# Kernel optimization log

Hardware: AMD Instinct MI355X
Metric: run time of the kernel (lower is better)

## Reference

```python
import jax, jax.numpy as jnp
import numpy as np

NEG_SLOPE = 0.2  # GAT LeakyReLU slope
EPS = 1e-16


def _pagat_conv(x, path_index, W, a, b, heads, out_ch, concat):
    """Path-augmented GAT conv: attention over (head, mid, tail) path triples,
    messages flow tail -> head, softmax-normalized per destination node."""
    N = x.shape[0]
    head, mid, tail = path_index[0], path_index[1], path_index[2]
    h = (x @ W).reshape(N, heads, out_ch)            # [N, H, C]
    # attention logits from all three path positions: [P, H]
    e = (jnp.einsum('phc,hc->ph', h[head], a[0])
         + jnp.einsum('phc,hc->ph', h[mid], a[1])
         + jnp.einsum('phc,hc->ph', h[tail], a[2]))
    e = jax.nn.leaky_relu(e, NEG_SLOPE)
    # segment softmax over paths grouped by destination (head) node
    m = jax.ops.segment_max(e, head, num_segments=N)  # [N, H]
    ex = jnp.exp(e - m[head])
    s = jax.ops.segment_sum(ex, head, num_segments=N)  # [N, H]
    alpha = ex / (s[head] + EPS)                       # [P, H]
    # aggregate tail features weighted by attention
    out = jax.ops.segment_sum(alpha[..., None] * h[tail], head, num_segments=N)  # [N, H, C]
    if concat:
        out = out.reshape(N, heads * out_ch)
    else:
        out = out.mean(axis=1)
    return out + b


def setup_inputs() -> dict:
    key = jax.random.key(0)
    ks = jax.random.split(key, 8)
    N, F_in, H, C, CLS, P = 100000, 500, 8, 16, 16, 1000000
    x = jax.random.normal(ks[0], (N, F_in), dtype=jnp.float32)
    path_index = jax.random.randint(ks[1], (3, P), 0, N, dtype=jnp.int32)
    W1 = jax.random.normal(ks[2], (F_in, H * C), dtype=jnp.float32) * 0.05
    a1 = jax.random.normal(ks[3], (3, H, C), dtype=jnp.float32) * 0.05
    b1 = jnp.zeros((H * C,), dtype=jnp.float32)
    W2 = jax.random.normal(ks[4], (H * C, CLS), dtype=jnp.float32) * 0.05
    a2 = jax.random.normal(ks[5], (3, 1, CLS), dtype=jnp.float32) * 0.05
    b2 = jnp.zeros((CLS,), dtype=jnp.float32)
    return {"x": x, "path_index": path_index, "W1": W1, "a1": a1, "b1": b1,
            "W2": W2, "a2": a2, "b2": b2}


def reference(x, path_index, W1, a1, b1, W2, a2, b2):
    # eval mode: dropout is identity
    h = _pagat_conv(x, path_index, W1, a1, b1, heads=8, out_ch=16, concat=True)
    h = jax.nn.elu(h)
    h = _pagat_conv(h, path_index, W2, a2, b2, heads=1, out_ch=16, concat=False)
    return jax.nn.log_softmax(h, axis=1)
```

## Files before the change

### kernel.cpp

```cpp
#include <hip/hip_runtime.h>
#include <hip/hip_bf16.h>

#define F_IN  500
#define HC    128
#define NHEAD 8
#define CDIM  16
#define NCLS  16
#define KPAD  512

static __device__ __forceinline__ float bf(const __hip_bfloat16 v) {
    return __bfloat162float(v);
}

static __device__ __forceinline__ unsigned int enc_f32(float f) {
    unsigned int u = __float_as_uint(f);
    return (u & 0x80000000u) ? ~u : (u | 0x80000000u);
}
static __device__ __forceinline__ float dec_f32(unsigned int u) {
    return __uint_as_float((u & 0x80000000u) ? (u & 0x7FFFFFFFu) : ~u);
}

typedef __bf16 bf16x8 __attribute__((ext_vector_type(8)));
typedef float f32x4 __attribute__((ext_vector_type(4)));

static __device__ __forceinline__ void gload16(const void* g, void* l) {
    __builtin_amdgcn_global_load_lds(
        (const __attribute__((address_space(1))) void*)g,
        (__attribute__((address_space(3))) void*)l, 16, 0, 0);
}

static __device__ __forceinline__ unsigned ldsoff(const void* p) {
    return (unsigned)(size_t)(const __attribute__((address_space(3))) void*)p;
}

static __device__ __forceinline__ void ds_read_f4(unsigned addr, float4& out) {
    asm volatile("ds_read_b128 %0, %1" : "=v"(out) : "v"(addr) : "memory");
}

template<int OFF>
static __device__ __forceinline__ bf16x8 gld_b(const __bf16* p) {
    bf16x8 o;
    asm volatile("global_load_dwordx4 %0, %1, off offset:%2"
                 : "=v"(o) : "v"(p), "i"(OFF) : "memory");
    return o;
}

__global__ void prep_kernel(const float* __restrict__ W1,
                            __bf16* __restrict__ w1t_hi,
                            __bf16* __restrict__ w1t_lo,
                            int* __restrict__ zp, int nz)
{
    int e = blockIdx.x * 256 + threadIdx.x;
    if (e < HC * KPAD) {
        int j = e & 7, lane = (e >> 3) & 63, ct = (e >> 9) & 3;
        int t = (e >> 11) & 15, wc = (e >> 15) & 1;
        int c = wc * 64 + ct * 16 + (lane & 15);
        int k = t * 32 + (lane >> 4) * 8 + j;
        float v = (k < F_IN) ? W1[k * HC + c] : 0.f;
        __bf16 h = (__bf16)v;
        w1t_hi[e] = h;
        w1t_lo[e] = (__bf16)(v - (float)h);
    }
    if (e < nz) zp[e] = 0;
}

static __device__ __forceinline__ void split8(const float4 a, const float4 b,
                                              bf16x8& hi, bf16x8& lo) {
    float v[8] = {a.x, a.y, a.z, a.w, b.x, b.y, b.z, b.w};
#pragma unroll
    for (int j = 0; j < 8; j++) {
        __bf16 h = (__bf16)v[j];
        hi[j] = h;
        lo[j] = (__bf16)(v[j] - (float)h);
    }
}

__global__ __launch_bounds__(256, 3) void gemm1_v7(
    const float* __restrict__ x,
    const __bf16* __restrict__ w1hi, const __bf16* __restrict__ w1lo,
    const float* __restrict__ zpad,
    __hip_bfloat16* __restrict__ h1,
    const int* __restrict__ pidx, int* __restrict__ deg, int N, int P)
{
    __shared__ float As[4][64 * 32];

    const int tid = threadIdx.x;
    const int lane = tid & 63, wave = tid >> 6;
    const int m = lane & 15, q = lane >> 4;
    const int wr = wave >> 1, wc = wave & 1;
    const int n0 = blockIdx.x * 64;
    const int woff = wave << 10;

    auto stage = [&](int buf, int t) {
        const int k0 = t * 32;
#pragma unroll
        for (int j = 0; j < 2; ++j) {
            int idx = j * 256 + tid;
            int r = idx >> 3, ps = idx & 7;
            int ls = ps ^ (r & 7);
            int kk = k0 + ls * 4;
            int grow = n0 + r;
            const float* src = (kk < F_IN)
                ? (x + (size_t)(grow < N ? grow : 0) * F_IN + kk)
                : zpad;
            gload16(src, (char*)&As[buf][0] + j * 4096 + woff);
        }
    };

    const __bf16* bh_base = w1hi + (size_t)wc * 32768 + (size_t)lane * 8;
    const __bf16* bl_base = w1lo + (size_t)wc * 32768 + (size_t)lane * 8;

    auto loadB = [&](bf16x8 (&bh)[4], bf16x8 (&bl)[4], int t) {
        const __bf16* ph = bh_base + (size_t)t * 2048;
        const __bf16* pl = bl_base + (size_t)t * 2048;
        bh[0] = gld_b<0>(ph);    bh[1] = gld_b<1024>(ph);
        bh[2] = gld_b<2048>(ph); bh[3] = gld_b<3072>(ph);
        bl[0] = gld_b<0>(pl);    bl[1] = gld_b<1024>(pl);
        bl[2] = gld_b<2048>(pl); bl[3] = gld_b<3072>(pl);
    };

    unsigned abase[4];
#pragma unroll
    for (int i = 0; i < 4; ++i) abase[i] = ldsoff(&As[i][0]);
    unsigned aoffs[2][2];
#pragma unroll
    for (int rt = 0; rt < 2; ++rt) {
        int r = wr * 32 + rt * 16 + m, x7 = r & 7;
        aoffs[rt][0] = r * 128 + (((2 * q) ^ x7) << 4);
        aoffs[rt][1] = r * 128 + (((2 * q + 1) ^ x7) << 4);
    }

    f32x4 acc[2][4];
#pragma unroll
    for (int rt = 0; rt < 2; ++rt)
#pragma unroll
        for (int ct = 0; ct < 4; ++ct) acc[rt][ct] = (f32x4){0.f, 0.f, 0.f, 0.f};

    bf16x8 bhA[4], blA[4], bhB[4], blB[4];

    stage(0, 0);
    stage(1, 1);
    loadB(bhA, blA, 0);
    stage(2, 2);

    auto compute = [&](bf16x8 (&bh)[4], bf16x8 (&bl)[4],
                       bf16x8 (&ah)[2], bf16x8 (&al)[2]) {
        __builtin_amdgcn_s_setprio(1);
#pragma unroll
        for (int rt = 0; rt < 2; ++rt)
#pragma unroll
            for (int ct = 0; ct < 4; ++ct) {
                acc[rt][ct] = __builtin_amdgcn_mfma_f32_16x16x32_bf16(ah[rt], bh[ct], acc[rt][ct], 0, 0, 0);
                acc[rt][ct] = __builtin_amdgcn_mfma_f32_16x16x32_bf16(ah[rt], bl[ct], acc[rt][ct], 0, 0, 0);
                acc[rt][ct] = __builtin_amdgcn_mfma_f32_16x16x32_bf16(al[rt], bh[ct], acc[rt][ct], 0, 0, 0);
            }
        __builtin_amdgcn_s_setprio(0);
    };

#pragma unroll
    for (int t = 0; t < 16; ++t) {
        if (t > 0) __builtin_amdgcn_s_barrier();
        if (t + 1 < 16) {
            if ((t & 1) == 0) loadB(bhB, blB, t + 1);
            else              loadB(bhA, blA, t + 1);
        }
        if (t + 3 < 16) stage((t + 3) & 3, t + 3);

        if (t <= 12)      asm volatile("s_waitcnt vmcnt(12)" ::: "memory");
        else if (t == 13) asm volatile("s_waitcnt vmcnt(10)" ::: "memory");
        else if (t == 14) asm volatile("s_waitcnt vmcnt(8)" ::: "memory");
        else              asm volatile("s_waitcnt vmcnt(0)" ::: "memory");
        __builtin_amdgcn_s_barrier();

        const int cur = t & 3;
        float4 fa[2][2];
        ds_read_f4(abase[cur] + aoffs[0][0], fa[0][0]);
        ds_read_f4(abase[cur] + aoffs[0][1], fa[0][1]);
        ds_read_f4(abase[cur] + aoffs[1][0], fa[1][0]);
        ds_read_f4(abase[cur] + aoffs[1][1], fa[1][1]);
        asm volatile("s_waitcnt lgkmcnt(0)" ::: "memory");
        __builtin_amdgcn_sched_barrier(0);

        bf16x8 ah[2], al[2];
        split8(fa[0][0], fa[0][1], ah[0], al[0]);
        split8(fa[1][0], fa[1][1], ah[1], al[1]);

        if ((t & 1) == 0) compute(bhA, blA, ah, al);
        else              compute(bhB, blB, ah, al);
    }

#pragma unroll
    for (int rt = 0; rt < 2; ++rt) {
        int rbase = n0 + wr * 32 + rt * 16 + q * 4;
#pragma unroll
        for (int ct = 0; ct < 4; ++ct) {
            int col = wc * 64 + ct * 16 + m;
#pragma unroll
            for (int r = 0; r < 4; ++r) {
                int row = rbase + r;
                if (row < N)
                    h1[(size_t)row * HC + col] = __float2bfloat16(acc[rt][ct][r]);
            }
        }
    }

    const int gsz = gridDim.x * 256;
    for (int i = blockIdx.x * 256 + tid; i < P; i += gsz)
        atomicAdd(deg + pidx[i], 1);
}

__global__ void dots1_kernel(const __hip_bfloat16* __restrict__ h1,
                             const float* __restrict__ a1,
                             float* __restrict__ d1,
                             unsigned int* __restrict__ gmax, int N)
{
    __shared__ unsigned int sm[16];
    if (threadIdx.x < 16) sm[threadIdx.x] = 0;
    __syncthreads();
    int id = blockIdx.x * blockDim.x + threadIdx.x;
    if (id < N * NHEAD) {
        int n = id >> 3, h = id & 7;
        const __hip_bfloat16* hp = h1 + (size_t)n * HC + h * CDIM;
        bf16x8 v0 = *(const bf16x8*)hp;
        bf16x8 v1 = *(const bf16x8*)(hp + 8);
        float s0 = 0.f, s1 = 0.f, s2 = 0.f;
#pragma unroll
        for (int c = 0; c < CDIM; c++) {
            float v = (c < 8) ? (float)v0[c & 7] : (float)v1[c & 7];
            s0 += v * a1[(0 * NHEAD + h) * CDIM + c];
            s1 += v * a1[(1 * NHEAD + h) * CDIM + c];
            s2 += v * a1[(2 * NHEAD + h) * CDIM + c];
        }
        d1[id] = s0;
        d1[N * NHEAD + id] = s1;
        d1[2 * N * NHEAD + id] = s2;
        atomicMax(&sm[h], enc_f32(s1));
        atomicMax(&sm[8 + h], enc_f32(s2));
    }
    __syncthreads();
    if (threadIdx.x < 16) atomicMax(&gmax[threadIdx.x], sm[threadIdx.x]);
}

__global__ void scan1_kernel(const int* __restrict__ deg, int* __restrict__ start,
                             int* __restrict__ bsum, int N) {
    __shared__ int sh[256];
    int i = blockIdx.x * 256 + threadIdx.x;
    int v = (i < N) ? deg[i] : 0;
    sh[threadIdx.x] = v;
    __syncthreads();
#pragma unroll
    for (int off = 1; off < 256; off <<= 1) {
        int x = (threadIdx.x >= off) ? sh[threadIdx.x - off] : 0;
        __syncthreads();
        sh[threadIdx.x] += x;
        __syncthreads();
    }
    if (i < N) start[i] = sh[threadIdx.x] - v;
    if (threadIdx.x == 255) bsum[blockIdx.x] = sh[255];
}

__global__ void scan2_kernel(int* __restrict__ bsum, int nb) {
    __shared__ int sh[512];
    int v = (threadIdx.x < nb) ? bsum[threadIdx.x] : 0;
    sh[threadIdx.x] = v;
    __syncthreads();
#pragma unroll
    for (int off = 1; off < 512; off <<= 1) {
        int x = (threadIdx.x >= off) ? sh[threadIdx.x - off] : 0;
        __syncthreads();
        sh[threadIdx.x] += x;
        __syncthreads();
    }
    if (threadIdx.x < nb) bsum[threadIdx.x] = sh[threadIdx.x] - v;
}

__global__ void scan3_kernel(int* __restrict__ start, const int* __restrict__ bsum, int N) {
    int i = blockIdx.x * 256 + threadIdx.x;
    if (i < N) start[i] += bsum[blockIdx.x];
}

__global__ void scatter_kernel(const int* __restrict__ pidx,
                               const int* __restrict__ start,
                               int* __restrict__ cursor,
                               int* __restrict__ csr, int P) {
    int p = blockIdx.x * blockDim.x + threadIdx.x;
    if (p >= P) return;
    int hd = pidx[p];
    int pos = atomicAdd(cursor + hd, 1);
    csr[start[hd] + pos] = p;
}

__global__ __launch_bounds__(256) void attn1_csr_kernel(
    const int* __restrict__ csr, const int* __restrict__ start,
    const int* __restrict__ deg, const int* __restrict__ pidx,
    const float* __restrict__ d1, const __hip_bfloat16* __restrict__ h1,
    const float* __restrict__ b1, const unsigned int* __restrict__ gmax,
    float* __restrict__ elu_out, int N, int P)
{
    int node = blockIdx.x * 4 + (threadIdx.x >> 6);
    if (node >= N) return;
    int lane = threadIdx.x & 63;
    int h = lane >> 3;
    int s0 = start[node], dg = deg[node];
    const float* d1m = d1 + (size_t)N * NHEAD;
    const float* d1t = d1 + (size_t)2 * N * NHEAD;
    const float dh = d1[node * NHEAD + h];
    float zub = dh + dec_f32(gmax[h]) + dec_f32(gmax[8 + h]);
    const float mxub = zub > 0.f ? zub : 0.2f * zub;

    float acc0 = 0.f, acc1 = 0.f, den = 0.f;
    for (int k0 = 0; k0 < dg; k0 += 8) {
        int kk = k0 + (lane & 7);
        bool valid = kk < dg;
        int p = csr[s0 + (valid ? kk : dg - 1)];
        int mid = pidx[P + p], tl = pidx[2 * P + p];
        float z = dh + d1m[mid * NHEAD + h] + d1t[tl * NHEAD + h];
        float e = z > 0.f ? z : 0.2f * z;
        float ex = valid ? __expf(e - mxub) : 0.f;
        den += ex;
        __hip_bfloat162 v[8];
        float exs[8];
#pragma unroll
        for (int dk = 0; dk < 8; dk++) {
            int tl_b = __shfl(tl, dk, 8);
            exs[dk] = __shfl(ex, dk, 8);
            v[dk] = *(const __hip_bfloat162*)(h1 + (size_t)tl_b * HC + 2 * lane);
        }
#pragma unroll
        for (int dk = 0; dk < 8; dk++) {
            acc0 += exs[dk] * bf(v[dk].x);
            acc1 += exs[dk] * bf(v[dk].y);
        }
    }
#pragma unroll
    for (int w = 1; w < 8; w <<= 1) den += __shfl_xor(den, w, 8);

    float inv = 1.f / (den + 1e-16f);
    int j0 = 2 * lane;
    float v0 = acc0 * inv + b1[j0];
    float v1 = acc1 * inv + b1[j0 + 1];
    v0 = v0 > 0.f ? v0 : __expf(v0) - 1.f;
    v1 = v1 > 0.f ? v1 : __expf(v1) - 1.f;
    *(float2*)(elu_out + (size_t)node * HC + j0) = make_float2(v0, v1);
}

__global__ __launch_bounds__(256) void layer2_kernel(
    const float* __restrict__ elu, const float* __restrict__ W2,
    const float* __restrict__ a2,
    float* __restrict__ h2, float* __restrict__ d2,
    unsigned int* __restrict__ gmax2, int N)
{
    __shared__ float rows[16][HC + 1];
    __shared__ float h2s[16][NCLS + 1];
    __shared__ unsigned int smax[2];
    const int n0 = blockIdx.x * 16;
    const int tid = threadIdx.x;
    if (tid < 2) smax[tid] = 0;
    for (int idx = tid; idx < 16 * HC; idx += 256) {
        int r = idx >> 7, c = idx & 127;
        rows[r][c] = (n0 + r < N) ? elu[(size_t)(n0 + r) * HC + c] : 0.f;
    }
    __syncthreads();
    int ln = tid >> 4, c = tid & 15;
    float acc = 0.f;
#pragma unroll 8
    for (int j = 0; j < HC; j++) acc += rows[ln][j] * W2[j * NCLS + c];
    h2s[ln][c] = acc;
    if (n0 + ln < N) h2[(size_t)(n0 + ln) * NCLS + c] = acc;
    __syncthreads();
    if (tid < 48) {
        int l = tid / 3, j = tid - l * 3;
        if (n0 + l < N) {
            float s = 0.f;
#pragma unroll
            for (int cc = 0; cc < NCLS; cc++) s += h2s[l][cc] * a2[j * NCLS + cc];
            d2[j * N + n0 + l] = s;
            if (j) atomicMax(&smax[j - 1], enc_f32(s));
        }
    }
    __syncthreads();
    if (tid < 2) atomicMax(&gmax2[tid], smax[tid]);
}

__global__ __launch_bounds__(256) void attn2_csr_kernel(
    const int* __restrict__ csr, const int* __restrict__ start,
    const int* __restrict__ deg, const int* __restrict__ pidx,
    const float* __restrict__ d2, const float* __restrict__ h2,
    const float* __restrict__ b2, const unsigned int* __restrict__ gmax2,
    float* __restrict__ out, int N, int P)
{
    int node = blockIdx.x * 16 + (threadIdx.x >> 4);
    if (node >= N) return;
    int c = threadIdx.x & 15;
    int s0 = start[node], dg = deg[node];
    const float dh = d2[node];
    const float* d2m = d2 + N;
    const float* d2t = d2 + 2 * N;
    float zub = dh + dec_f32(gmax2[0]) + dec_f32(gmax2[1]);
    const float mxub = zub > 0.f ? zub : 0.2f * zub;

    float acc = 0.f, den = 0.f;
    for (int k0 = 0; k0 < dg; k0 += 16) {
        int kk = k0 + c;
        bool valid = kk < dg;
        int p = csr[s0 + (valid ? kk : dg - 1)];
        int mid = pidx[P + p], tl = pidx[2 * P + p];
        float z = dh + d2m[mid] + d2t[tl];
        float e = z > 0.f ? z : 0.2f * z;
        float ex = valid ? __expf(e - mxub) : 0.f;
        den += ex;
        float vv[16], exs[16];
#pragma unroll
        for (int dk = 0; dk < 16; dk++) {
            int tl_b = __shfl(tl, dk, 16);
            exs[dk] = __shfl(ex, dk, 16);
            vv[dk] = h2[(size_t)tl_b * NCLS + c];
        }
#pragma unroll
        for (int dk = 0; dk < 16; dk++) acc += exs[dk] * vv[dk];
    }
#pragma unroll
    for (int w = 1; w < 16; w <<= 1) den += __shfl_xor(den, w, 16);

    float o = acc / (den + 1e-16f) + b2[c];
    float m2 = o;
#pragma unroll
    for (int w = 1; w < 16; w <<= 1) m2 = fmaxf(m2, __shfl_xor(m2, w, 16));
    float ex = __expf(o - m2), sm = ex;
#pragma unroll
    for (int w = 1; w < 16; w <<= 1) sm += __shfl_xor(sm, w, 16);
    float r = o - m2 - __logf(sm);
    out[(size_t)node * NCLS + c] = r;
}

extern "C" void kernel_launch(void* const* d_in, const int* in_sizes, int n_in,
                              void* d_out, int out_size, void* d_ws, size_t ws_size,
                              hipStream_t stream)
{
    const float* x  = (const float*)d_in[0];
    const int*   pi = (const int*)d_in[1];
    const float* W1 = (const float*)d_in[2];
    const float* a1 = (const float*)d_in[3];
    const float* b1 = (const float*)d_in[4];
    const float* W2 = (const float*)d_in[5];
    const float* a2 = (const float*)d_in[6];
    const float* b2 = (const float*)d_in[7];

    const int N = in_sizes[0] / F_IN;
    const int P = in_sizes[1] / 3;

    float* ws = (float*)d_ws;
    size_t off_h1     = 0;
    size_t off_d1     = (size_t)64 * N;
    size_t off_elu    = (size_t)88 * N;
    size_t off_h2     = (size_t)216 * N;
    size_t off_d2     = (size_t)232 * N;
    size_t off_deg    = (size_t)235 * N;
    size_t off_start  = (size_t)236 * N;
    size_t off_cursor = (size_t)237 * N;
    size_t off_gmax   = (size_t)238 * N;
    size_t off_zpad   = (size_t)238 * N + 32;
    size_t off_bsum   = (size_t)238 * N + 96;
    size_t off_csr    = (size_t)238 * N + 96 + 1024;
    size_t off_w1th   = off_csr + P;
    size_t off_w1tl   = off_w1th + 32768;

    __hip_bfloat16* h1 = (__hip_bfloat16*)(ws + off_h1);
    float* d1   = ws + off_d1;
    float* elu  = ws + off_elu;
    float* h2   = ws + off_h2;
    float* d2   = ws + off_d2;
    int* deg    = (int*)(ws + off_deg);
    int* start  = (int*)(ws + off_start);
    int* cursor = (int*)(ws + off_cursor);
    unsigned int* gmax  = (unsigned int*)(ws + off_gmax);
    unsigned int* gmax2 = (unsigned int*)(ws + off_gmax) + 16;
    float* zpad = ws + off_zpad;
    int* bsum   = (int*)(ws + off_bsum);
    int* csr    = (int*)(ws + off_csr);
    __bf16* w1t_hi = (__bf16*)(ws + off_w1th);
    __bf16* w1t_lo = (__bf16*)(ws + off_w1tl);

    const int BLK = 256;
    const int nb = (N + 255) / 256;
    const int nz = 3 * N + 96;
    const int nprep = (HC * KPAD > nz ? HC * KPAD : nz);

    prep_kernel<<<(nprep + 255) / 256, 256, 0, stream>>>(W1, w1t_hi, w1t_lo, deg, nz);
    gemm1_v7<<<(N + 63) / 64, 256, 0, stream>>>(x, w1t_hi, w1t_lo, zpad, h1, pi, deg, N, P);
    dots1_kernel<<<(N * NHEAD + BLK - 1) / BLK, BLK, 0, stream>>>(h1, a1, d1, gmax, N);
    scan1_kernel<<<nb, 256, 0, stream>>>(deg, start, bsum, N);
    scan2_kernel<<<1, 512, 0, stream>>>(bsum, nb);
    scan3_kernel<<<nb, 256, 0, stream>>>(start, bsum, N);
    scatter_kernel<<<(P + BLK - 1) / BLK, BLK, 0, stream>>>(pi, start, cursor, csr, P);
    attn1_csr_kernel<<<(N + 3) / 4, 256, 0, stream>>>(csr, start, deg, pi, d1, h1, b1, gmax, elu, N, P);
    layer2_kernel<<<(N + 15) / 16, 256, 0, stream>>>(elu, W2, a2, h2, d2, gmax2, N);
    attn2_csr_kernel<<<(N + 15) / 16, 256, 0, stream>>>(csr, start, deg, pi, d2, h2, b2, gmax2,
                                                        (float*)d_out, N, P);
}
```

Measured before the change: 675.2 us.

## Fuse attention dot products into GEMM1 epilogue and widen layer2 row tiles

Moves the per-head attention logit dot products (d1) and their global maxima out of a separate kernel and into the GEMM1 epilogue. They are computed from the accumulators, rounded to bf16, and reduced with 16-lane shuffles. This removes one launch and a full re-read of h1. Layer2 now processes 64 rows per block instead of 16, with float4 loads, to amortize W2 reads and reduce block count. The cost is extra shuffle work and register pressure in the GEMM epilogue, and more shared memory in layer2.

Result: faster. 611.5 us (-9.4%).

```diff
diff --git a/kernel.cpp b/kernel.cpp
--- a/kernel.cpp
+++ b/kernel.cpp
@@ -75,14 +75,17 @@
     }
 }
 
-__global__ __launch_bounds__(256, 3) void gemm1_v7(
+__global__ __launch_bounds__(256, 3) void gemm1_v8(
     const float* __restrict__ x,
     const __bf16* __restrict__ w1hi, const __bf16* __restrict__ w1lo,
     const float* __restrict__ zpad,
     __hip_bfloat16* __restrict__ h1,
+    const float* __restrict__ a1, float* __restrict__ d1,
+    unsigned int* __restrict__ gmax,
     const int* __restrict__ pidx, int* __restrict__ deg, int N, int P)
 {
     __shared__ float As[4][64 * 32];
+    __shared__ unsigned int smax[16];
 
     const int tid = threadIdx.x;
     const int lane = tid & 63, wave = tid >> 6;
@@ -90,6 +93,8 @@
     const int wr = wave >> 1, wc = wave & 1;
     const int n0 = blockIdx.x * 64;
     const int woff = wave << 10;
+
+    if (tid < 16) smax[tid] = 0;
 
     auto stage = [&](int buf, int t) {
         const int k0 = t * 32;
@@ -204,41 +209,40 @@
         }
     }
 
+#pragma unroll
+    for (int rt = 0; rt < 2; ++rt)
+#pragma unroll
+        for (int ct = 0; ct < 4; ++ct) {
+            int h = wc * 4 + ct;
+            float w0 = a1[(0 * NHEAD + h) * CDIM + m];
+            float w1 = a1[(1 * NHEAD + h) * CDIM + m];
+            float w2 = a1[(2 * NHEAD + h) * CDIM + m];
+#pragma unroll
+            for (int r = 0; r < 4; ++r) {
+                float v = bf(__float2bfloat16(acc[rt][ct][r]));
+                float s0 = v * w0, s1 = v * w1, s2 = v * w2;
+#pragma unroll
+                for (int w = 1; w < 16; w <<= 1) {
+                    s0 += __shfl_xor(s0, w, 16);
+                    s1 += __shfl_xor(s1, w, 16);
+                    s2 += __shfl_xor(s2, w, 16);
+                }
+                int row = n0 + wr * 32 + rt * 16 + q * 4 + r;
+                if (m == 0 && row < N) {
+                    d1[(size_t)row * NHEAD + h] = s0;
+                    d1[(size_t)N * NHEAD + (size_t)row * NHEAD + h] = s1;
+                    d1[(size_t)2 * N * NHEAD + (size_t)row * NHEAD + h] = s2;
+                    atomicMax(&smax[h], enc_f32(s1));
+                    atomicMax(&smax[8 + h], enc_f32(s2));
+                }
+            }
+        }
+    __syncthreads();
+    if (tid < 16) atomicMax(&gmax[tid], smax[tid]);
+
     const int gsz = gridDim.x * 256;
     for (int i = blockIdx.x * 256 + tid; i < P; i += gsz)
         atomicAdd(deg + pidx[i], 1);
-}
-
-__global__ void dots1_kernel(const __hip_bfloat16* __restrict__ h1,
-                             const float* __restrict__ a1,
-                             float* __restrict__ d1,
-                             unsigned int* __restrict__ gmax, int N)
-{
-    __shared__ unsigned int sm[16];
-    if (threadIdx.x < 16) sm[threadIdx.x] = 0;
-    __syncthreads();
-    int id = blockIdx.x * blockDim.x + threadIdx.x;
-    if (id < N * NHEAD) {
-        int n = id >> 3, h = id & 7;
-        const __hip_bfloat16* hp = h1 + (size_t)n * HC + h * CDIM;
-        bf16x8 v0 = *(const bf16x8*)hp;
-        bf16x8 v1 = *(const bf16x8*)(hp + 8);
-        float s0 = 0.f, s1 = 0.f, s2 = 0.f;
-#pragma unroll
-        for (int c = 0; c < CDIM; c++) {
-            float v = (c < 8) ? (float)v0[c & 7] : (float)v1[c & 7];
-            s0 += v * a1[(0 * NHEAD + h) * CDIM + c];
-            s1 += v * a1[(1 * NHEAD + h) * CDIM + c];
-            s2 += v * a1[(2 * NHEAD + h) * CDIM + c];
-        }
-        d1[id] = s0;
-        d1[N * NHEAD + id] = s1;
-        d1[2 * N * NHEAD + id] = s2;
-        atomicMax(&sm[h], enc_f32(s1));
-        atomicMax(&sm[8 + h], enc_f32(s2));
-    }
-    __syncthreads();
-    if (threadIdx.x < 16) atomicMax(&gmax[threadIdx.x], sm[threadIdx.x]);
 }
 
 __global__ void scan1_kernel(const int* __restrict__ deg, int* __restrict__ start,
@@ -350,25 +354,32 @@
     float* __restrict__ h2, float* __restrict__ d2,
     unsigned int* __restrict__ gmax2, int N)
 {
-    __shared__ float rows[16][HC + 1];
-    __shared__ float h2s[16][NCLS + 1];
+    __shared__ float rows[64][HC + 4];
+    __shared__ float h2s[64][NCLS + 1];
     __shared__ unsigned int smax[2];
-    const int n0 = blockIdx.x * 16;
+    const int n0 = blockIdx.x * 64;
     const int tid = threadIdx.x;
     if (tid < 2) smax[tid] = 0;
-    for (int idx = tid; idx < 16 * HC; idx += 256) {
-        int r = idx >> 7, c = idx & 127;
-        rows[r][c] = (n0 + r < N) ? elu[(size_t)(n0 + r) * HC + c] : 0.f;
+    for (int idx = tid; idx < 64 * 32; idx += 256) {
+        int r = idx >> 5, c4 = idx & 31;
+        float4 v = (n0 + r < N)
+            ? *(const float4*)&elu[(size_t)(n0 + r) * HC + c4 * 4]
+            : make_float4(0.f, 0.f, 0.f, 0.f);
+        *(float4*)&rows[r][c4 * 4] = v;
     }
     __syncthreads();
     int ln = tid >> 4, c = tid & 15;
-    float acc = 0.f;
+#pragma unroll
+    for (int pass = 0; pass < 4; ++pass) {
+        int r = pass * 16 + ln;
+        float acc = 0.f;
 #pragma unroll 8
-    for (int j = 0; j < HC; j++) acc += rows[ln][j] * W2[j * NCLS + c];
-    h2s[ln][c] = acc;
-    if (n0 + ln < N) h2[(size_t)(n0 + ln) * NCLS + c] = acc;
+        for (int j = 0; j < HC; j++) acc += rows[r][j] * W2[j * NCLS + c];
+        h2s[r][c] = acc;
+        if (n0 + r < N) h2[(size_t)(n0 + r) * NCLS + c] = acc;
+    }
     __syncthreads();
-    if (tid < 48) {
+    if (tid < 192) {
         int l = tid / 3, j = tid - l * 3;
         if (n0 + l < N) {
             float s = 0.f;
@@ -487,14 +498,14 @@
     const int nprep = (HC * KPAD > nz ? HC * KPAD : nz);
 
     prep_kernel<<<(nprep + 255) / 256, 256, 0, stream>>>(W1, w1t_hi, w1t_lo, deg, nz);
-    gemm1_v7<<<(N + 63) / 64, 256, 0, stream>>>(x, w1t_hi, w1t_lo, zpad, h1, pi, deg, N, P);
-    dots1_kernel<<<(N * NHEAD + BLK - 1) / BLK, BLK, 0, stream>>>(h1, a1, d1, gmax, N);
+    gemm1_v8<<<(N + 63) / 64, 256, 0, stream>>>(x, w1t_hi, w1t_lo, zpad, h1,
+                                                a1, d1, gmax, pi, deg, N, P);
     scan1_kernel<<<nb, 256, 0, stream>>>(deg, start, bsum, N);
     scan2_kernel<<<1, 512, 0, stream>>>(bsum, nb);
     scan3_kernel<<<nb, 256, 0, stream>>>(start, bsum, N);
     scatter_kernel<<<(P + BLK - 1) / BLK, BLK, 0, stream>>>(pi, start, cursor, csr, P);
     attn1_csr_kernel<<<(N + 3) / 4, 256, 0, stream>>>(csr, start, deg, pi, d1, h1, b1, gmax, elu, N, P);
-    layer2_kernel<<<(N + 15) / 16, 256, 0, stream>>>(elu, W2, a2, h2, d2, gmax2, N);
+    layer2_kernel<<<(N + 63) / 64, 256, 0, stream>>>(elu, W2, a2, h2, d2, gmax2, N);
     attn2_csr_kernel<<<(N + 15) / 16, 256, 0, stream>>>(csr, start, deg, pi, d2, h2, b2, gmax2,
                                                         (float*)d_out, N, P);
 }
```
